# Optimization experiments

Hardware: AMD Instinct MI355X
Metric: run time of the kernel (lower is better)

Reference implementation:

```python
import jax, jax.numpy as jnp
import numpy as np

B, T, D, V, E = 128, 256, 1024, 32000, 300


def setup_inputs() -> dict:
    key = jax.random.key(0)
    ks = jax.random.split(key, 9)
    s = lambda d: 1.0 / np.sqrt(d)
    return {
        "input_to_decoder": jax.random.randint(ks[0], (B, 1), 0, V),
        "encoder_output": jax.random.normal(ks[1], (B, T, D), jnp.float32) * s(D),
        "state_h": jax.random.normal(ks[2], (B, D), jnp.float32) * s(D),
        "state_c": jax.random.normal(ks[3], (B, D), jnp.float32) * s(D),
        "emb_table": jax.random.normal(ks[4], (V, E), jnp.float32) * 0.02,
        "W_lstm": jax.random.normal(ks[5], (D + E, 4 * D), jnp.float32) * s(D + E),
        "U_lstm": jax.random.normal(ks[6], (D, 4 * D), jnp.float32) * s(D),
        "b_lstm": jnp.zeros((4 * D,), jnp.float32),
        "W_dense": jax.random.normal(ks[7], (D, V), jnp.float32) * s(D),
        "b_dense": jnp.zeros((V,), jnp.float32),
    }


def reference(input_to_decoder, encoder_output, state_h, state_c,
              emb_table, W_lstm, U_lstm, b_lstm, W_dense, b_dense):
    # embedding lookup + squeeze(axis=1): [B,1] -> [B,E]
    emb = emb_table[input_to_decoder[:, 0]]
    # Bahdanau-style dot scores: [B,T]
    scores = jnp.einsum("btd,bd->bt", encoder_output, state_h)
    # NOTE: faithful to source - context uses RAW (pre-softmax) scores
    context = jnp.einsum("btd,bt->bd", encoder_output, scores)  # [B,D]
    attention_weights = jax.nn.softmax(scores, axis=1)[..., None]  # [B,T,1]
    # concat context + embedding, single LSTM cell step (Keras gate order i,f,g,o)
    x = jnp.concatenate([context, emb], axis=1)  # [B,D+E]
    z = x @ W_lstm + state_h @ U_lstm + b_lstm  # [B,4D]
    zi, zf, zg, zo = jnp.split(z, 4, axis=1)
    c_new = jax.nn.sigmoid(zf) * state_c + jax.nn.sigmoid(zi) * jnp.tanh(zg)
    h_new = jax.nn.sigmoid(zo) * jnp.tanh(c_new)
    logits = h_new @ W_dense + b_dense  # [B,V]
    return logits, h_new, c_new, attention_weights, context
```

## Files before the change

kernel.cpp:

```cpp
#include <hip/hip_runtime.h>
#include <hip/hip_bf16.h>
#include <cmath>


#define Bc 128
#define Tc 256
#define Dc 1024
#define Vc 32000
#define Ec 300
#define KREAL 2348
#define KXP 2688
#define KSPLIT 7
#define N4 4096

typedef __attribute__((ext_vector_type(8))) short bf16x8;
typedef __attribute__((ext_vector_type(4))) float f32x4;

static __device__ __forceinline__ short f2bf(float x) {
    __hip_bfloat16 b = __float2bfloat16(x);
    return *reinterpret_cast<short*>(&b);
}
static __device__ __forceinline__ unsigned pack2(float a, float b) {
    return (unsigned)(unsigned short)f2bf(a) | ((unsigned)(unsigned short)f2bf(b) << 16);
}

__global__ void k_att1(const float* __restrict__ enc, const float* __restrict__ h,
                       float* __restrict__ scores_g, float* __restrict__ ctx_part) {
    const int tc = blockIdx.x;
    const int b  = blockIdx.y;
    const int tid = threadIdx.x;
    const int wave = tid >> 6, lane = tid & 63;
    __shared__ float s_acc[4][1024];

    const float4* h4 = (const float4*)(h + ((size_t)b << 10));
    float4 hv0 = h4[lane], hv1 = h4[lane + 64], hv2 = h4[lane + 128], hv3 = h4[lane + 192];

    float4 a0 = {0,0,0,0}, a1 = {0,0,0,0}, a2 = {0,0,0,0}, a3 = {0,0,0,0};
    const int t0 = (tc << 6) + (wave << 4);
    const float4* e4 = (const float4*)(enc + ((size_t)(b * Tc + t0) << 10));

    #pragma unroll 2
    for (int i = 0; i < 16; ++i) {
        float4 e0 = e4[lane], e1 = e4[lane + 64], e2 = e4[lane + 128], e3 = e4[lane + 192];
        e4 += 256;
        float d = e0.x*hv0.x + e0.y*hv0.y + e0.z*hv0.z + e0.w*hv0.w
                + e1.x*hv1.x + e1.y*hv1.y + e1.z*hv1.z + e1.w*hv1.w
                + e2.x*hv2.x + e2.y*hv2.y + e2.z*hv2.z + e2.w*hv2.w
                + e3.x*hv3.x + e3.y*hv3.y + e3.z*hv3.z + e3.w*hv3.w;
        #pragma unroll
        for (int off = 32; off; off >>= 1) d += __shfl_xor(d, off, 64);
        if (lane == 0) scores_g[(b << 8) + t0 + i] = d;
        a0.x += d*e0.x; a0.y += d*e0.y; a0.z += d*e0.z; a0.w += d*e0.w;
        a1.x += d*e1.x; a1.y += d*e1.y; a1.z += d*e1.z; a1.w += d*e1.w;
        a2.x += d*e2.x; a2.y += d*e2.y; a2.z += d*e2.z; a2.w += d*e2.w;
        a3.x += d*e3.x; a3.y += d*e3.y; a3.z += d*e3.z; a3.w += d*e3.w;
    }

    *(float4*)&s_acc[wave][lane << 2]         = a0;
    *(float4*)&s_acc[wave][256 + (lane << 2)] = a1;
    *(float4*)&s_acc[wave][512 + (lane << 2)] = a2;
    *(float4*)&s_acc[wave][768 + (lane << 2)] = a3;
    __syncthreads();
    float4 r0 = *(const float4*)&s_acc[0][tid << 2];
    float4 r1 = *(const float4*)&s_acc[1][tid << 2];
    float4 r2 = *(const float4*)&s_acc[2][tid << 2];
    float4 r3 = *(const float4*)&s_acc[3][tid << 2];
    float4 r;
    r.x = r0.x + r1.x + r2.x + r3.x;
    r.y = r0.y + r1.y + r2.y + r3.y;
    r.z = r0.z + r1.z + r2.z + r3.z;
    r.w = r0.w + r1.w + r2.w + r3.w;
    *(float4*)(ctx_part + (((size_t)(tc << 7) + b) << 10) + (tid << 2)) = r;
}

__global__ void k_att2(const float* __restrict__ ctx_part, const float* __restrict__ scores_g,
                       const int* __restrict__ idx, const float* __restrict__ emb_table,
                       const float* __restrict__ h,
                       float* __restrict__ ctx_out, float* __restrict__ attn_out,
                       unsigned short* __restrict__ x_bf) {
    const int b = blockIdx.x;
    const int tid = threadIdx.x;
    __shared__ float red[256];

    float4 cv = {0.f, 0.f, 0.f, 0.f};
    #pragma unroll
    for (int tc = 0; tc < 4; ++tc) {
        float4 s = *(const float4*)(ctx_part + (((size_t)(tc << 7) + b) << 10) + (tid << 2));
        cv.x += s.x; cv.y += s.y; cv.z += s.z; cv.w += s.w;
    }
    *(float4*)(ctx_out + ((size_t)b << 10) + (tid << 2)) = cv;

    unsigned short* xb = x_bf + (size_t)b * KXP;
    uint2 p0; p0.x = pack2(cv.x, cv.y); p0.y = pack2(cv.z, cv.w);
    *(uint2*)&xb[tid << 2] = p0;

    int row = idx[b];
    for (int i = tid; i < Ec; i += 256)
        xb[Dc + i] = (unsigned short)f2bf(emb_table[(size_t)row * Ec + i]);

    float4 hv = *(const float4*)(h + ((size_t)b << 10) + (tid << 2));
    uint2 p1; p1.x = pack2(hv.x, hv.y); p1.y = pack2(hv.z, hv.w);
    *(uint2*)&xb[(Dc + Ec) + (tid << 2)] = p1;

    for (int i = tid; i < KXP - KREAL; i += 256) xb[KREAL + i] = 0;

    float v = scores_g[(b << 8) + tid];
    red[tid] = v;
    __syncthreads();
    for (int s = 128; s; s >>= 1) { if (tid < s) red[tid] = fmaxf(red[tid], red[tid + s]); __syncthreads(); }
    float m = red[0];
    __syncthreads();
    float e = __expf(v - m);
    red[tid] = e;
    __syncthreads();
    for (int s = 128; s; s >>= 1) { if (tid < s) red[tid] += red[tid + s]; __syncthreads(); }
    attn_out[(b << 8) + tid] = e / red[0];
}

__global__ __launch_bounds__(512) void k_zgemm_mfma(
        const unsigned short* __restrict__ xbf, const float* __restrict__ Wl,
        const float* __restrict__ Ul, float* __restrict__ z_part) {
    __shared__ __align__(16) short blds[2 * 8 * 64 * 8];
    const int tid  = threadIdx.x;
    const int wid  = tid >> 6;
    const int lane = tid & 63;
    const int g    = lane >> 4;
    const int r    = lane & 15;
    const int n0   = blockIdx.x << 6;
    const int ksp  = blockIdx.y;

    const int pr = tid >> 4;
    const int c  = tid & 15;
    const int kk = (pr << 1) & 31;
    const int gg = kk >> 3, jj = kk & 7;
    const int ks0 = pr >> 4;

    f32x4 acc[4] = {};
    const unsigned short* xrow = xbf + (size_t)((wid << 4) + r) * KXP;

    float4 wra[2], wrb[2];
    bf16x8 areg[2][2];

    auto loadWU = [&](int gk) -> float4 {
        if (gk < 1324) return *(const float4*)(Wl + (size_t)gk * N4 + n0 + (c << 2));
        if (gk < KREAL) return *(const float4*)(Ul + (size_t)(gk - 1324) * N4 + n0 + (c << 2));
        return float4{0.f, 0.f, 0.f, 0.f};
    };

    {
        const int kt = (ksp * 6) << 6;
        wra[0] = loadWU(kt + (pr << 1));
        wrb[0] = loadWU(kt + (pr << 1) + 1);
        areg[0][0] = *(const bf16x8*)&xrow[kt + (g << 3)];
        areg[0][1] = *(const bf16x8*)&xrow[kt + 32 + (g << 3)];
    }

    #pragma unroll
    for (int t = 0; t < 6; ++t) {
        const int cur = t & 1;
        const int coff = cur << 12;
        {
            const float av[4] = {wra[cur].x, wra[cur].y, wra[cur].z, wra[cur].w};
            const float bv[4] = {wrb[cur].x, wrb[cur].y, wrb[cur].z, wrb[cur].w};
            #pragma unroll
            for (int i = 0; i < 4; ++i) {
                int n = (c << 2) + i;
                int nt = n >> 4;
                int inner = (gg << 4) | (n & 15);
                int Xs = ((((ks0 << 2) + nt) << 6) | inner) ^ nt;
                *(unsigned*)&blds[coff + (Xs << 3) + jj] = pack2(av[i], bv[i]);
            }
        }
        if (t < 5) {
            const int kt = ((ksp * 6) + t + 1) << 6;
            wra[cur ^ 1] = loadWU(kt + (pr << 1));
            wrb[cur ^ 1] = loadWU(kt + (pr << 1) + 1);
            areg[cur ^ 1][0] = *(const bf16x8*)&xrow[kt + (g << 3)];
            areg[cur ^ 1][1] = *(const bf16x8*)&xrow[kt + 32 + (g << 3)];
        }
        __syncthreads();
        #pragma unroll
        for (int ks = 0; ks < 2; ++ks) {
            #pragma unroll
            for (int nt = 0; nt < 4; ++nt) {
                int Xs = ((((ks << 2) + nt) << 6) | lane) ^ nt;
                bf16x8 bfr = *(const bf16x8*)&blds[coff + (Xs << 3)];
                acc[nt] = __builtin_amdgcn_mfma_f32_16x16x32_bf16(areg[cur][ks], bfr, acc[nt], 0, 0, 0);
            }
        }
    }

    float* zp = z_part + ((size_t)ksp << 19);
    #pragma unroll
    for (int nt = 0; nt < 4; ++nt) {
        int col = n0 + (nt << 4) + r;
        #pragma unroll
        for (int j = 0; j < 4; ++j) {
            int rowm = (wid << 4) + (g << 2) + j;
            zp[((size_t)rowm << 12) + col] = acc[nt][j];
        }
    }
}

__global__ void k_gates(const float* __restrict__ z_part, const float* __restrict__ b_lstm,
                        const float* __restrict__ c_in, float* __restrict__ h_new,
                        float* __restrict__ c_new, unsigned short* __restrict__ h_bf) {
    int i = blockIdx.x * 256 + threadIdx.x;
    int b = i >> 10, d = i & 1023;
    size_t base = ((size_t)b << 12) + d;
    float zi = b_lstm[d], zf = b_lstm[d + 1024], zg = b_lstm[d + 2048], zo = b_lstm[d + 3072];
    #pragma unroll
    for (int ks = 0; ks < KSPLIT; ++ks) {
        const float* zp = z_part + ((size_t)ks << 19);
        zi += zp[base];
        zf += zp[base + 1024];
        zg += zp[base + 2048];
        zo += zp[base + 3072];
    }
    float si = 1.f / (1.f + __expf(-zi));
    float sf = 1.f / (1.f + __expf(-zf));
    float so = 1.f / (1.f + __expf(-zo));
    float cn = sf * c_in[i] + si * tanhf(zg);
    float hn = so * tanhf(cn);
    c_new[i] = cn;
    h_new[i] = hn;
    h_bf[i] = (unsigned short)f2bf(hn);
}

__global__ __launch_bounds__(512) void k_logits_mfma(
        const unsigned short* __restrict__ hbf, const float* __restrict__ Wd,
        const float* __restrict__ bd, float* __restrict__ out) {
    __shared__ __align__(16) short blds[2 * 16 * 64 * 8];
    const int tid  = threadIdx.x;
    const int wid  = tid >> 6;
    const int lane = tid & 63;
    const int g    = lane >> 4;
    const int r    = lane & 15;
    const int n0   = blockIdx.x << 6;

    const int pr = tid >> 4;
    const int c  = tid & 15;
    const int kk = (pr << 1) & 31;
    const int gg = kk >> 3, jj = kk & 7;
    const int ksA = pr >> 4;
    const int ksB = ksA + 2;

    f32x4 acc[4] = {};
    const unsigned short* hrow = hbf + ((size_t)((wid << 4) + r) << 10);
    const float* wbase = Wd + (size_t)(pr << 1) * Vc + n0 + (c << 2);

    float4 wra[2], wrb[2], wrc[2], wrd[2];
    bf16x8 areg[2][4];

    {
        wra[0] = *(const float4*)(wbase);
        wrb[0] = *(const float4*)(wbase + Vc);
        wrc[0] = *(const float4*)(wbase + (size_t)64 * Vc);
        wrd[0] = *(const float4*)(wbase + (size_t)65 * Vc);
        #pragma unroll
        for (int ks = 0; ks < 4; ++ks)
            areg[0][ks] = *(const bf16x8*)&hrow[(ks << 5) + (g << 3)];
    }

    #pragma unroll
    for (int t = 0; t < 8; ++t) {
        const int cur = t & 1;
        const int coff = cur << 13;
        {
            const float a0[4] = {wra[cur].x, wra[cur].y, wra[cur].z, wra[cur].w};
            const float b0[4] = {wrb[cur].x, wrb[cur].y, wrb[cur].z, wrb[cur].w};
            const float c0[4] = {wrc[cur].x, wrc[cur].y, wrc[cur].z, wrc[cur].w};
            const float d0[4] = {wrd[cur].x, wrd[cur].y, wrd[cur].z, wrd[cur].w};
            #pragma unroll
            for (int i = 0; i < 4; ++i) {
                int n = (c << 2) + i;
                int nt = n >> 4;
                int inner = (gg << 4) | (n & 15);
                int XsA = ((((ksA << 2) + nt) << 6) | inner) ^ nt;
                int XsB = ((((ksB << 2) + nt) << 6) | inner) ^ nt;
                *(unsigned*)&blds[coff + (XsA << 3) + jj] = pack2(a0[i], b0[i]);
                *(unsigned*)&blds[coff + (XsB << 3) + jj] = pack2(c0[i], d0[i]);
            }
        }
        if (t < 7) {
            const float* wb2 = wbase + (size_t)((t + 1) << 7) * Vc;
            wra[cur ^ 1] = *(const float4*)(wb2);
            wrb[cur ^ 1] = *(const float4*)(wb2 + Vc);
            wrc[cur ^ 1] = *(const float4*)(wb2 + (size_t)64 * Vc);
            wrd[cur ^ 1] = *(const float4*)(wb2 + (size_t)65 * Vc);
            #pragma unroll
            for (int ks = 0; ks < 4; ++ks)
                areg[cur ^ 1][ks] = *(const bf16x8*)&hrow[((t + 1) << 7) + (ks << 5) + (g << 3)];
        }
        __syncthreads();
        #pragma unroll
        for (int ks = 0; ks < 4; ++ks) {
            #pragma unroll
            for (int nt = 0; nt < 4; ++nt) {
                int Xs = ((((ks << 2) + nt) << 6) | lane) ^ nt;
                bf16x8 bfr = *(const bf16x8*)&blds[coff + (Xs << 3)];
                acc[nt] = __builtin_amdgcn_mfma_f32_16x16x32_bf16(areg[cur][ks], bfr, acc[nt], 0, 0, 0);
            }
        }
    }

    #pragma unroll
    for (int nt = 0; nt < 4; ++nt) {
        int col = n0 + (nt << 4) + r;
        float bias = bd[col];
        #pragma unroll
        for (int j = 0; j < 4; ++j) {
            int row = (wid << 4) + (g << 2) + j;
            out[(size_t)row * Vc + col] = acc[nt][j] + bias;
        }
    }
}

extern "C" void kernel_launch(void* const* d_in, const int* in_sizes, int n_in,
                              void* d_out, int out_size, void* d_ws, size_t ws_size,
                              hipStream_t stream) {
    const int*   idx = (const int*)d_in[0];
    const float* enc = (const float*)d_in[1];
    const float* h   = (const float*)d_in[2];
    const float* c   = (const float*)d_in[3];
    const float* emb = (const float*)d_in[4];
    const float* Wl  = (const float*)d_in[5];
    const float* Ul  = (const float*)d_in[6];
    const float* bl  = (const float*)d_in[7];
    const float* Wd  = (const float*)d_in[8];
    const float* bd  = (const float*)d_in[9];

    float* out    = (float*)d_out;
    float* logits = out;
    float* h_new  = out + 4096000;
    float* c_new  = out + 4227072;
    float* attn   = out + 4358144;
    float* ctx    = out + 4390912;

    float*          ctx_part = out;
    float*          scores_g = out + 524288;
    float*          z_part   = out;
    unsigned short* x_bf16   = (unsigned short*)d_ws;
    unsigned short* h_bf16   = (unsigned short*)d_ws + 344064;

    hipLaunchKernelGGL(k_att1, dim3(4, 128), dim3(256), 0, stream, enc, h, scores_g, ctx_part);
    hipLaunchKernelGGL(k_att2, dim3(128), dim3(256), 0, stream, ctx_part, scores_g, idx, emb, h,
                       ctx, attn, x_bf16);
    hipLaunchKernelGGL(k_zgemm_mfma, dim3(64, KSPLIT), dim3(512), 0, stream, x_bf16, Wl, Ul, z_part);
    hipLaunchKernelGGL(k_gates, dim3(512), dim3(256), 0, stream, z_part, bl, c, h_new, c_new, h_bf16);
    hipLaunchKernelGGL(k_logits_mfma, dim3(500), dim3(512), 0, stream, h_bf16, Wd, bd, logits);
}
```

Baseline: 91.15 us.

## Reduce LSTM split-K to 4, vectorize gates kernel, add trailing barriers

Lowers the K-split of the LSTM gate GEMM from 7 to 4 chunks, each covering 11 tiles, and pads K to 2816. This cuts the partial-sum traffic and the reduction work in the gates kernel, at the cost of fewer blocks and a longer serial loop per block. The gates kernel now processes four elements per thread with float4 loads and stores and a packed bf16 write. The logits kernel gets a launch_bounds occupancy hint. Both MFMA loops gain a trailing __syncthreads, which closes a possible LDS double-buffer race but adds a barrier per iteration.

```diff
diff --git a/kernel.cpp b/kernel.cpp
--- a/kernel.cpp
+++ b/kernel.cpp
@@ -9,8 +9,8 @@
 #define Vc 32000
 #define Ec 300
 #define KREAL 2348
-#define KXP 2688
-#define KSPLIT 7
+#define KXP 2816
+#define KSPLIT 4
 #define N4 4096
 
 typedef __attribute__((ext_vector_type(8))) short bf16x8;
@@ -148,7 +148,7 @@
     };
 
     {
-        const int kt = (ksp * 6) << 6;
+        const int kt = (ksp * 11) << 6;
         wra[0] = loadWU(kt + (pr << 1));
         wrb[0] = loadWU(kt + (pr << 1) + 1);
         areg[0][0] = *(const bf16x8*)&xrow[kt + (g << 3)];
@@ -156,7 +156,7 @@
     }
 
     #pragma unroll
-    for (int t = 0; t < 6; ++t) {
+    for (int t = 0; t < 11; ++t) {
         const int cur = t & 1;
         const int coff = cur << 12;
         {
@@ -171,8 +171,8 @@
                 *(unsigned*)&blds[coff + (Xs << 3) + jj] = pack2(av[i], bv[i]);
             }
         }
-        if (t < 5) {
-            const int kt = ((ksp * 6) + t + 1) << 6;
+        if (t < 10) {
+            const int kt = ((ksp * 11) + t + 1) << 6;
             wra[cur ^ 1] = loadWU(kt + (pr << 1));
             wrb[cur ^ 1] = loadWU(kt + (pr << 1) + 1);
             areg[cur ^ 1][0] = *(const bf16x8*)&xrow[kt + (g << 3)];
@@ -188,6 +188,7 @@
                 acc[nt] = __builtin_amdgcn_mfma_f32_16x16x32_bf16(areg[cur][ks], bfr, acc[nt], 0, 0, 0);
             }
         }
+        __syncthreads();
     }
 
     float* zp = z_part + ((size_t)ksp << 19);
@@ -206,28 +207,40 @@
                         const float* __restrict__ c_in, float* __restrict__ h_new,
                         float* __restrict__ c_new, unsigned short* __restrict__ h_bf) {
     int i = blockIdx.x * 256 + threadIdx.x;
-    int b = i >> 10, d = i & 1023;
-    size_t base = ((size_t)b << 12) + d;
-    float zi = b_lstm[d], zf = b_lstm[d + 1024], zg = b_lstm[d + 2048], zo = b_lstm[d + 3072];
+    int b = i >> 8, d4 = (i & 255) << 2;
+    size_t base = ((size_t)b << 12) + d4;
+    float4 zi = *(const float4*)(b_lstm + d4);
+    float4 zf = *(const float4*)(b_lstm + d4 + 1024);
+    float4 zg = *(const float4*)(b_lstm + d4 + 2048);
+    float4 zo = *(const float4*)(b_lstm + d4 + 3072);
     #pragma unroll
     for (int ks = 0; ks < KSPLIT; ++ks) {
         const float* zp = z_part + ((size_t)ks << 19);
-        zi += zp[base];
-        zf += zp[base + 1024];
-        zg += zp[base + 2048];
-        zo += zp[base + 3072];
-    }
-    float si = 1.f / (1.f + __expf(-zi));
-    float sf = 1.f / (1.f + __expf(-zf));
-    float so = 1.f / (1.f + __expf(-zo));
-    float cn = sf * c_in[i] + si * tanhf(zg);
-    float hn = so * tanhf(cn);
-    c_new[i] = cn;
-    h_new[i] = hn;
-    h_bf[i] = (unsigned short)f2bf(hn);
-}
-
-__global__ __launch_bounds__(512) void k_logits_mfma(
+        float4 t;
+        t = *(const float4*)(zp + base);        zi.x += t.x; zi.y += t.y; zi.z += t.z; zi.w += t.w;
+        t = *(const float4*)(zp + base + 1024); zf.x += t.x; zf.y += t.y; zf.z += t.z; zf.w += t.w;
+        t = *(const float4*)(zp + base + 2048); zg.x += t.x; zg.y += t.y; zg.z += t.z; zg.w += t.w;
+        t = *(const float4*)(zp + base + 3072); zo.x += t.x; zo.y += t.y; zo.z += t.z; zo.w += t.w;
+    }
+    float4 cin = *(const float4*)(c_in + ((size_t)b << 10) + d4);
+    float4 cn, hn;
+    {
+        float si = 1.f/(1.f+__expf(-zi.x)), sf = 1.f/(1.f+__expf(-zf.x)), so = 1.f/(1.f+__expf(-zo.x));
+        cn.x = sf*cin.x + si*tanhf(zg.x); hn.x = so*tanhf(cn.x);
+        si = 1.f/(1.f+__expf(-zi.y)); sf = 1.f/(1.f+__expf(-zf.y)); so = 1.f/(1.f+__expf(-zo.y));
+        cn.y = sf*cin.y + si*tanhf(zg.y); hn.y = so*tanhf(cn.y);
+        si = 1.f/(1.f+__expf(-zi.z)); sf = 1.f/(1.f+__expf(-zf.z)); so = 1.f/(1.f+__expf(-zo.z));
+        cn.z = sf*cin.z + si*tanhf(zg.z); hn.z = so*tanhf(cn.z);
+        si = 1.f/(1.f+__expf(-zi.w)); sf = 1.f/(1.f+__expf(-zf.w)); so = 1.f/(1.f+__expf(-zo.w));
+        cn.w = sf*cin.w + si*tanhf(zg.w); hn.w = so*tanhf(cn.w);
+    }
+    *(float4*)(c_new + ((size_t)b << 10) + d4) = cn;
+    *(float4*)(h_new + ((size_t)b << 10) + d4) = hn;
+    uint2 hp; hp.x = pack2(hn.x, hn.y); hp.y = pack2(hn.z, hn.w);
+    *(uint2*)&h_bf[((size_t)b << 10) + d4] = hp;
+}
+
+__global__ __launch_bounds__(512, 4) void k_logits_mfma(
         const unsigned short* __restrict__ hbf, const float* __restrict__ Wd,
         const float* __restrict__ bd, float* __restrict__ out) {
     __shared__ __align__(16) short blds[2 * 16 * 64 * 8];
@@ -302,6 +315,7 @@
                 acc[nt] = __builtin_amdgcn_mfma_f32_16x16x32_bf16(areg[cur][ks], bfr, acc[nt], 0, 0, 0);
             }
         }
+        __syncthreads();
     }
 
     #pragma unroll
@@ -341,12 +355,12 @@
     float*          scores_g = out + 524288;
     float*          z_part   = out;
     unsigned short* x_bf16   = (unsigned short*)d_ws;
-    unsigned short* h_bf16   = (unsigned short*)d_ws + 344064;
+    unsigned short* h_bf16   = (unsigned short*)d_ws + 360448;
 
     hipLaunchKernelGGL(k_att1, dim3(4, 128), dim3(256), 0, stream, enc, h, scores_g, ctx_part);
     hipLaunchKernelGGL(k_att2, dim3(128), dim3(256), 0, stream, ctx_part, scores_g, idx, emb, h,
                        ctx, attn, x_bf16);
     hipLaunchKernelGGL(k_zgemm_mfma, dim3(64, KSPLIT), dim3(512), 0, stream, x_bf16, Wl, Ul, z_part);
-    hipLaunchKernelGGL(k_gates, dim3(512), dim3(256), 0, stream, z_part, bl, c, h_new, c_new, h_bf16);
+    hipLaunchKernelGGL(k_gates, dim3(128), dim3(256), 0, stream, z_part, bl, c, h_new, c_new, h_bf16);
     hipLaunchKernelGGL(k_logits_mfma, dim3(500), dim3(512), 0, stream, h_bf16, Wd, bd, logits);
 }
```

Measured after the change: 97.35 us. 6.8% more time.
